# Optimization experiments

Hardware: AMD Instinct MI355X
Metric: run time of the kernel (lower is better)

## Reference

```python
import jax, jax.numpy as jnp
import numpy as np

N_NODES = 100000
N_EDGES = 3200000
VM, VA, PG, QG, PD, QD = 0, 1, 2, 3, 4, 5
G, B = 0, 1


def setup_inputs() -> dict:
    key = jax.random.key(0)
    k1, k2, k3, k4, k5 = jax.random.split(key, 5)
    pred = jax.random.normal(k1, (N_NODES, 6), dtype=jnp.float32)
    target = jax.random.normal(k2, (N_NODES, 6), dtype=jnp.float32)
    edge_index = jax.random.randint(k3, (2, N_EDGES), 0, N_NODES, dtype=jnp.int64)
    edge_attr = jax.random.normal(k4, (N_EDGES, 2), dtype=jnp.float32)
    mask = jax.random.randint(k5, (N_NODES, 6), 0, 2) == 1
    return {"pred": pred, "target": target, "edge_index": edge_index,
            "edge_attr": edge_attr, "mask": mask}


def reference(pred, target, edge_index, edge_attr, mask):
    # temp_pred[~mask] = target[~mask]
    temp_pred = jnp.where(mask, pred, target)
    vm = temp_pred[:, VM]
    va = temp_pred[:, VA]
    pg = temp_pred[:, PG]
    qg = temp_pred[:, QG]
    pd = temp_pred[:, PD]
    qd = temp_pred[:, QD]
    g = edge_attr[:, G]
    b = edge_attr[:, B]
    src, dst = edge_index[0], edge_index[1]

    v_from = vm[src]                      # [E] gather
    v_to = vm[dst]
    ang = va[src] - va[dst]
    c, s = jnp.cos(ang), jnp.sin(ang)
    vv = v_from * v_to
    p_flow = vv * (g * c + b * s)         # [E]
    q_flow = vv * (g * s - b * c)

    # scatter-add flows into source nodes
    p_calc = jax.ops.segment_sum(p_flow, src, num_segments=N_NODES)
    q_calc = jax.ops.segment_sum(q_flow, src, num_segments=N_NODES)

    p_imb = pg - pd - p_calc
    q_imb = qg - qd - q_calc
    loss = jnp.mean(p_imb ** 2) + jnp.mean(q_imb ** 2)
    return loss
```

## Files before the change

### kernel.cpp

```cpp
#include <hip/hip_runtime.h>
#include <cstdint>

#define N_NODES 100000
#define N_EDGES 3200000
#define SPAN    256
#define SHIFT   8
#define NB      ((N_NODES + SPAN - 1) / SPAN)
#define CHUNK   4096
#define NITER   (CHUNK / 256)
#define NBLK_A  ((N_EDGES + CHUNK - 1) / CHUNK)
#define K_MAX   12288

#define FP_SCALE 4096.0f
#define FP_INV   (1.0f / 4096.0f)

__global__ __launch_bounds__(256)
void prep_kernel(const float* __restrict__ pred,
                 const float* __restrict__ target,
                 const void* __restrict__ mask,
                 float2* __restrict__ u_tab,
                 float2* __restrict__ base_pq,
                 unsigned long long* __restrict__ ovf,
                 uint32_t* __restrict__ gcursor,
                 float* __restrict__ d_out, int out_size) {
    __shared__ int s_mask8;
    if (threadIdx.x < 64) {
        uint32_t w = ((const uint32_t*)mask)[threadIdx.x];
        bool nz = (w & 0xFFFFFF00u) != 0u;
        unsigned long long m = __ballot(nz);
        if (threadIdx.x == 0) s_mask8 = (m != 0ull) ? 1 : 0;
    }
    if (blockIdx.x == 0) {
        for (int b = threadIdx.x; b < NB; b += 256) gcursor[b] = 0u;
        if (threadIdx.x == 0)
            for (int k = 0; k < out_size; ++k) d_out[k] = 0.0f;
    }
    __syncthreads();

    int i = blockIdx.x * 256 + threadIdx.x;
    if (i >= N_NODES) return;

    const float2* p2 = (const float2*)pred;
    const float2* t2 = (const float2*)target;
    float2 pa = p2[3 * i], pb = p2[3 * i + 1], pc = p2[3 * i + 2];
    float2 ta = t2[3 * i], tb = t2[3 * i + 1], tc = t2[3 * i + 2];
    float pr[6] = {pa.x, pa.y, pb.x, pb.y, pc.x, pc.y};
    float tg[6] = {ta.x, ta.y, tb.x, tb.y, tc.x, tc.y};
    int mk[6];
    if (s_mask8) {
        const uint16_t* mu = (const uint16_t*)mask;
        uint16_t m0 = mu[3 * i], m1 = mu[3 * i + 1], m2 = mu[3 * i + 2];
        mk[0] = m0 & 0xFF; mk[1] = m0 >> 8;
        mk[2] = m1 & 0xFF; mk[3] = m1 >> 8;
        mk[4] = m2 & 0xFF; mk[5] = m2 >> 8;
    } else {
        const int2* mi = (const int2*)mask;
        int2 m0 = mi[3 * i], m1 = mi[3 * i + 1], m2 = mi[3 * i + 2];
        mk[0] = m0.x; mk[1] = m0.y; mk[2] = m1.x;
        mk[3] = m1.y; mk[4] = m2.x; mk[5] = m2.y;
    }
    float tp[6];
    #pragma unroll
    for (int j = 0; j < 6; ++j) tp[j] = mk[j] ? pr[j] : tg[j];

    float s, c;
    sincosf(tp[1], &s, &c);
    u_tab[i]   = make_float2(tp[0] * c, tp[0] * s);
    base_pq[i] = make_float2(tp[2] - tp[4], tp[3] - tp[5]);
    ovf[i] = 0ull;
}

__global__ __launch_bounds__(256)
void bin_kernel(const void* __restrict__ edge_index,
                const float2* __restrict__ edge_attr,
                const float2* __restrict__ u_tab,
                uint32_t* __restrict__ gcursor,
                uint2* __restrict__ recs,
                unsigned long long* __restrict__ ovf,
                int k_cap) {
    __shared__ uint2 s_rec[CHUNK];
    __shared__ uint32_t s_cnt[NB];
    __shared__ uint32_t s_pref[NB + 1];
    __shared__ uint32_t s_gbase[NB];
    __shared__ int s_i64;

    uint32_t* scanA = (uint32_t*)s_rec;
    uint32_t* scanB = scanA + 512;

    const int tid = threadIdx.x;
    if (tid < 64) {
        uint32_t w = ((const uint32_t*)edge_index)[tid];
        bool nz = (tid & 1) && (w != 0u);
        unsigned long long m = __ballot(nz);
        if (tid == 0) s_i64 = (m == 0ull) ? 1 : 0;
    }
    for (int b = tid; b < NB; b += 256) s_cnt[b] = 0u;
    __syncthreads();
    const bool is64 = (s_i64 != 0);
    const int ebase = blockIdx.x * CHUNK;
    const int nE = min(CHUNK, N_EDGES - ebase);

    uint32_t src_r[NITER];
    #pragma unroll
    for (int it = 0; it < NITER; ++it) {
        int j = it * 256 + tid;
        uint32_t s = 0u;
        if (j < nE) {
            int e = ebase + j;
            s = is64 ? (uint32_t)((const unsigned long long*)edge_index)[e]
                     : ((const uint32_t*)edge_index)[e];
            atomicAdd(&s_cnt[s >> SHIFT], 1u);
        }
        src_r[it] = s;
    }
    __syncthreads();

    {
        scanA[tid]       = (tid < NB) ? s_cnt[tid] : 0u;
        scanA[tid + 256] = (tid + 256 < NB) ? s_cnt[tid + 256] : 0u;
        __syncthreads();
        uint32_t* sa = scanA; uint32_t* sb = scanB;
        for (int off = 1; off < 512; off <<= 1) {
            #pragma unroll
            for (int h = 0; h < 2; ++h) {
                int k = h * 256 + tid;
                uint32_t v = sa[k];
                if (k >= off) v += sa[k - off];
                sb[k] = v;
            }
            __syncthreads();
            uint32_t* t = sa; sa = sb; sb = t;
        }
        if (tid == 0) s_pref[0] = 0u;
        for (int b = tid; b < NB; b += 256) s_pref[b + 1] = sa[b];
        __syncthreads();
    }

    for (int b = tid; b < NB; b += 256) {
        uint32_t cnt = s_pref[b + 1] - s_pref[b];
        s_gbase[b] = cnt ? atomicAdd(&gcursor[b], cnt) : 0u;
        s_cnt[b] = 0u;
    }
    __syncthreads();

    #pragma unroll
    for (int it = 0; it < NITER; ++it) {
        int j = it * 256 + tid;
        if (j < nE) {
            int e = ebase + j;
            uint32_t dst = is64
                ? (uint32_t)((const unsigned long long*)edge_index)[(size_t)N_EDGES + e]
                : ((const uint32_t*)edge_index)[(size_t)N_EDGES + e];
            float2 gb = edge_attr[e];
            float2 u  = u_tab[dst];
            float vr = gb.x * u.x - gb.y * u.y;
            float vi = -(gb.y * u.x + gb.x * u.y);
            uint32_t nid = src_r[it];
            uint32_t bk = nid >> SHIFT, lid = nid & (SPAN - 1);
            uint32_t r = atomicAdd(&s_cnt[bk], 1u);
            uint2 rc;
            rc.x = (__float_as_uint(vr) & ~0xFFu) | lid;
            rc.y = __float_as_uint(vi);
            s_rec[s_pref[bk] + r] = rc;
        }
    }
    __syncthreads();

    for (int slot = tid; slot < nE; slot += 256) {
        int lo = 0, hi = NB;
        while (hi - lo > 1) {
            int mid = (lo + hi) >> 1;
            if (s_pref[mid] <= (uint32_t)slot) lo = mid; else hi = mid;
        }
        int bk = lo;
        uint32_t pos = s_gbase[bk] + ((uint32_t)slot - s_pref[bk]);
        uint2 rc = s_rec[slot];
        if ((int)pos < k_cap) {
            recs[(size_t)bk * k_cap + pos] = rc;
        } else {
            float vr = __uint_as_float(rc.x & ~0xFFu);
            float vi = __uint_as_float(rc.y);
            uint32_t nid = ((uint32_t)bk << SHIFT) | (rc.x & 0xFFu);
            int pi = __float2int_rn(vr * FP_SCALE);
            int qi = __float2int_rn(vi * FP_SCALE);
            unsigned long long enc =
                ((unsigned long long)(long long)pi << 32) +
                (unsigned long long)(unsigned int)qi;
            atomicAdd(&ovf[nid], enc);
        }
    }
}

__global__ __launch_bounds__(1024)
void reduce_kernel(const uint2* __restrict__ recs,
                   const uint32_t* __restrict__ gcursor,
                   const float2* __restrict__ u_tab,
                   const float2* __restrict__ base_pq,
                   const unsigned long long* __restrict__ ovf,
                   float* __restrict__ d_out, int k_cap) {
    __shared__ float2 s_acc[SPAN];
    __shared__ float s_part[16];
    if (threadIdx.x < SPAN) s_acc[threadIdx.x] = make_float2(0.0f, 0.0f);
    __syncthreads();

    const int b = blockIdx.x;
    const int n = min((int)gcursor[b], k_cap);
    const uint2* r = recs + (size_t)b * k_cap;
    for (int j = threadIdx.x; j < n; j += 1024) {
        uint2 rc = r[j];
        uint32_t lid = rc.x & 0xFFu;
        atomicAdd(&s_acc[lid].x, __uint_as_float(rc.x & ~0xFFu));
        atomicAdd(&s_acc[lid].y, __uint_as_float(rc.y));
    }
    __syncthreads();

    float v = 0.0f;
    int node = b * SPAN + (int)threadIdx.x;
    if (threadIdx.x < SPAN && node < N_NODES) {
        float2 S = s_acc[threadIdx.x];
        unsigned long long u = ovf[node];
        if (u) {
            int qs = (int)(unsigned int)(u & 0xFFFFFFFFull);
            long long rem = (long long)(u - (unsigned long long)(long long)qs);
            int ps = (int)(rem >> 32);
            S.x += (float)ps * FP_INV;
            S.y += (float)qs * FP_INV;
        }
        float2 ui = u_tab[node];
        float2 bp = base_pq[node];
        float pc = ui.x * S.x - ui.y * S.y;
        float qc = ui.x * S.y + ui.y * S.x;
        float p = bp.x - pc, q = bp.y - qc;
        v = p * p + q * q;
    }
    #pragma unroll
    for (int off = 32; off > 0; off >>= 1) v += __shfl_down(v, off, 64);
    if ((threadIdx.x & 63) == 0) s_part[threadIdx.x >> 6] = v;
    __syncthreads();
    if (threadIdx.x == 0) {
        float t = 0.0f;
        #pragma unroll
        for (int w = 0; w < 16; ++w) t += s_part[w];
        atomicAdd(d_out, t * (1.0f / (float)N_NODES));
    }
}

extern "C" void kernel_launch(void* const* d_in, const int* in_sizes, int n_in,
                              void* d_out, int out_size, void* d_ws, size_t ws_size,
                              hipStream_t stream) {
    const float*  pred       = (const float*)d_in[0];
    const float*  target     = (const float*)d_in[1];
    const void*   edge_index = d_in[2];
    const float2* edge_attr  = (const float2*)d_in[3];
    const void*   mask       = d_in[4];
    float* out = (float*)d_out;

    char* ws = (char*)d_ws;
    float2*             u_tab   = (float2*)ws;
    float2*             base_pq = (float2*)(ws + 800000);
    unsigned long long* ovf     = (unsigned long long*)(ws + 1600000);
    uint32_t*           gcursor = (uint32_t*)(ws + 2400000);
    uint2*              recs    = (uint2*)(ws + 2404096);

    long long avail = (long long)ws_size - 2404096;
    long long kc = (avail > 0) ? (avail / ((long long)NB * 8)) : 0;
    int k_cap = (int)((kc > K_MAX) ? K_MAX : kc);

    prep_kernel<<<(N_NODES + 255) / 256, 256, 0, stream>>>(
        pred, target, mask, u_tab, base_pq, ovf, gcursor, out, out_size);

    bin_kernel<<<NBLK_A, 256, 0, stream>>>(
        edge_index, edge_attr, u_tab, gcursor, recs, ovf, k_cap);

    reduce_kernel<<<NB, 1024, 0, stream>>>(
        recs, gcursor, u_tab, base_pq, ovf, out, k_cap);
}
```

Before: 201.8 us.

## Widen bin kernel, wave-shuffle scan, embed bucket id, replicate reduce accumulators

The bin kernel now runs 512 threads per block, and its multi-pass shared-memory prefix scan over bucket counts becomes a two-level wave-shuffle scan. Each record stores its bucket id in the low 9 bits of the imaginary field, so the scatter phase reads the bucket directly instead of binary-searching the prefix array. The reduce kernel spreads its shared float atomics across four replicated accumulator arrays to cut contention. The cost is 9 fewer mantissa bits on the imaginary component, and the scan assumes NB is at most 512.

```diff
diff --git a/kernel.cpp b/kernel.cpp
--- a/kernel.cpp
+++ b/kernel.cpp
@@ -7,7 +7,8 @@
 #define SHIFT   8
 #define NB      ((N_NODES + SPAN - 1) / SPAN)
 #define CHUNK   4096
-#define NITER   (CHUNK / 256)
+#define BTHREADS 512
+#define NITER   (CHUNK / BTHREADS)
 #define NBLK_A  ((N_EDGES + CHUNK - 1) / CHUNK)
 #define K_MAX   12288
 
@@ -70,7 +71,7 @@
     ovf[i] = 0ull;
 }
 
-__global__ __launch_bounds__(256)
+__global__ __launch_bounds__(BTHREADS)
 void bin_kernel(const void* __restrict__ edge_index,
                 const float2* __restrict__ edge_attr,
                 const float2* __restrict__ u_tab,
@@ -82,19 +83,18 @@
     __shared__ uint32_t s_cnt[NB];
     __shared__ uint32_t s_pref[NB + 1];
     __shared__ uint32_t s_gbase[NB];
+    __shared__ uint32_t s_wsum[8], s_woff[8];
     __shared__ int s_i64;
 
-    uint32_t* scanA = (uint32_t*)s_rec;
-    uint32_t* scanB = scanA + 512;
-
     const int tid = threadIdx.x;
+    const int lane = tid & 63, wid = tid >> 6;
     if (tid < 64) {
         uint32_t w = ((const uint32_t*)edge_index)[tid];
         bool nz = (tid & 1) && (w != 0u);
         unsigned long long m = __ballot(nz);
         if (tid == 0) s_i64 = (m == 0ull) ? 1 : 0;
     }
-    for (int b = tid; b < NB; b += 256) s_cnt[b] = 0u;
+    if (tid < NB) s_cnt[tid] = 0u;
     __syncthreads();
     const bool is64 = (s_i64 != 0);
     const int ebase = blockIdx.x * CHUNK;
@@ -103,7 +103,7 @@
     uint32_t src_r[NITER];
     #pragma unroll
     for (int it = 0; it < NITER; ++it) {
-        int j = it * 256 + tid;
+        int j = it * BTHREADS + tid;
         uint32_t s = 0u;
         if (j < nE) {
             int e = ebase + j;
@@ -116,36 +116,41 @@
     __syncthreads();
 
     {
-        scanA[tid]       = (tid < NB) ? s_cnt[tid] : 0u;
-        scanA[tid + 256] = (tid + 256 < NB) ? s_cnt[tid + 256] : 0u;
+        uint32_t v0 = (tid < NB) ? s_cnt[tid] : 0u;
+        uint32_t x = v0;
+        #pragma unroll
+        for (int off = 1; off < 64; off <<= 1) {
+            uint32_t y = (uint32_t)__shfl_up((int)x, off, 64);
+            if (lane >= off) x += y;
+        }
+        if (lane == 63) s_wsum[wid] = x;
         __syncthreads();
-        uint32_t* sa = scanA; uint32_t* sb = scanB;
-        for (int off = 1; off < 512; off <<= 1) {
+        if (tid < 8) {
+            uint32_t w0 = s_wsum[tid];
+            uint32_t xx = w0;
             #pragma unroll
-            for (int h = 0; h < 2; ++h) {
-                int k = h * 256 + tid;
-                uint32_t v = sa[k];
-                if (k >= off) v += sa[k - off];
-                sb[k] = v;
+            for (int off = 1; off < 8; off <<= 1) {
+                uint32_t y = (uint32_t)__shfl_up((int)xx, off, 64);
+                if (tid >= off) xx += y;
             }
-            __syncthreads();
-            uint32_t* t = sa; sa = sb; sb = t;
-        }
+            s_woff[tid] = xx - w0;
+        }
+        __syncthreads();
+        uint32_t incl = x + s_woff[wid];
+        if (tid < NB) s_pref[tid + 1] = incl;
         if (tid == 0) s_pref[0] = 0u;
-        for (int b = tid; b < NB; b += 256) s_pref[b + 1] = sa[b];
+        if (tid < NB) {
+            uint32_t excl = incl - v0;
+            s_gbase[tid] = v0 ? atomicAdd(&gcursor[tid], v0) : 0u;
+            s_cnt[tid] = 0u;
+            (void)excl;
+        }
         __syncthreads();
     }
 
-    for (int b = tid; b < NB; b += 256) {
-        uint32_t cnt = s_pref[b + 1] - s_pref[b];
-        s_gbase[b] = cnt ? atomicAdd(&gcursor[b], cnt) : 0u;
-        s_cnt[b] = 0u;
-    }
-    __syncthreads();
-
     #pragma unroll
     for (int it = 0; it < NITER; ++it) {
-        int j = it * 256 + tid;
+        int j = it * BTHREADS + tid;
         if (j < nE) {
             int e = ebase + j;
             uint32_t dst = is64
@@ -160,27 +165,22 @@
             uint32_t r = atomicAdd(&s_cnt[bk], 1u);
             uint2 rc;
             rc.x = (__float_as_uint(vr) & ~0xFFu) | lid;
-            rc.y = __float_as_uint(vi);
+            rc.y = (__float_as_uint(vi) & ~0x1FFu) | bk;
             s_rec[s_pref[bk] + r] = rc;
         }
     }
     __syncthreads();
 
-    for (int slot = tid; slot < nE; slot += 256) {
-        int lo = 0, hi = NB;
-        while (hi - lo > 1) {
-            int mid = (lo + hi) >> 1;
-            if (s_pref[mid] <= (uint32_t)slot) lo = mid; else hi = mid;
-        }
-        int bk = lo;
+    for (int slot = tid; slot < nE; slot += BTHREADS) {
+        uint2 rc = s_rec[slot];
+        uint32_t bk = rc.y & 0x1FFu;
         uint32_t pos = s_gbase[bk] + ((uint32_t)slot - s_pref[bk]);
-        uint2 rc = s_rec[slot];
         if ((int)pos < k_cap) {
             recs[(size_t)bk * k_cap + pos] = rc;
         } else {
             float vr = __uint_as_float(rc.x & ~0xFFu);
-            float vi = __uint_as_float(rc.y);
-            uint32_t nid = ((uint32_t)bk << SHIFT) | (rc.x & 0xFFu);
+            float vi = __uint_as_float(rc.y & ~0x1FFu);
+            uint32_t nid = (bk << SHIFT) | (rc.x & 0xFFu);
             int pi = __float2int_rn(vr * FP_SCALE);
             int qi = __float2int_rn(vi * FP_SCALE);
             unsigned long long enc =
@@ -198,26 +198,35 @@
                    const float2* __restrict__ base_pq,
                    const unsigned long long* __restrict__ ovf,
                    float* __restrict__ d_out, int k_cap) {
-    __shared__ float2 s_acc[SPAN];
+    __shared__ float2 s_acc[4][SPAN];
     __shared__ float s_part[16];
-    if (threadIdx.x < SPAN) s_acc[threadIdx.x] = make_float2(0.0f, 0.0f);
+    if (threadIdx.x < SPAN) {
+        #pragma unroll
+        for (int r = 0; r < 4; ++r) s_acc[r][threadIdx.x] = make_float2(0.0f, 0.0f);
+    }
     __syncthreads();
 
     const int b = blockIdx.x;
     const int n = min((int)gcursor[b], k_cap);
+    const int rep = (threadIdx.x >> 6) & 3;
     const uint2* r = recs + (size_t)b * k_cap;
     for (int j = threadIdx.x; j < n; j += 1024) {
         uint2 rc = r[j];
         uint32_t lid = rc.x & 0xFFu;
-        atomicAdd(&s_acc[lid].x, __uint_as_float(rc.x & ~0xFFu));
-        atomicAdd(&s_acc[lid].y, __uint_as_float(rc.y));
+        atomicAdd(&s_acc[rep][lid].x, __uint_as_float(rc.x & ~0xFFu));
+        atomicAdd(&s_acc[rep][lid].y, __uint_as_float(rc.y & ~0x1FFu));
     }
     __syncthreads();
 
     float v = 0.0f;
     int node = b * SPAN + (int)threadIdx.x;
     if (threadIdx.x < SPAN && node < N_NODES) {
-        float2 S = s_acc[threadIdx.x];
+        float2 S = make_float2(0.0f, 0.0f);
+        #pragma unroll
+        for (int rr = 0; rr < 4; ++rr) {
+            float2 t = s_acc[rr][threadIdx.x];
+            S.x += t.x; S.y += t.y;
+        }
         unsigned long long u = ovf[node];
         if (u) {
             int qs = (int)(unsigned int)(u & 0xFFFFFFFFull);
@@ -269,7 +278,7 @@
     prep_kernel<<<(N_NODES + 255) / 256, 256, 0, stream>>>(
         pred, target, mask, u_tab, base_pq, ovf, gcursor, out, out_size);
 
-    bin_kernel<<<NBLK_A, 256, 0, stream>>>(
+    bin_kernel<<<NBLK_A, BTHREADS, 0, stream>>>(
         edge_index, edge_attr, u_tab, gcursor, recs, ovf, k_cap);
 
     reduce_kernel<<<NB, 1024, 0, stream>>>(
```

Result: no change. 198.5 us (-1.6%).
